# Performance work log

Hardware: AMD Instinct MI355X
Metric: run time of the kernel (lower is better)

The kernel has to match this reference:

```python
import jax, jax.numpy as jnp
import numpy as np

B, E, H, T = 32768, 64, 128, 12  # batch, embedding_dim, decoder_h_dim, pred_len


def setup_inputs() -> dict:
    key = jax.random.key(0)
    ks = jax.random.split(key, 13)
    f = lambda k, shape: jax.random.normal(k, shape, dtype=jnp.float32) * 0.05
    return {
        "last_pos": f(ks[0], (B, 2)),
        "last_pos_rel": f(ks[1], (B, 2)),
        "h0": f(ks[2], (1, B, H)),
        "c0": f(ks[3], (1, B, H)),
        "pred_ped_speed": jax.random.uniform(ks[4], (T, B, 1), dtype=jnp.float32),
        # spatial_embedding: Linear(3, E)
        "W_se": f(ks[5], (E, 3)),
        "b_se": f(ks[6], (E,)),
        # single-layer LSTM(E -> H), torch gate order [i, f, g, o]
        "W_ih": f(ks[7], (4 * H, E)),
        "W_hh": f(ks[8], (4 * H, H)),
        "b_ih": f(ks[9], (4 * H,)),
        "b_hh": f(ks[10], (4 * H,)),
        # hidden2pos: Linear(H, 2)
        "W_hp": f(ks[11], (2, H)),
        "b_hp": f(ks[12], (2,)),
    }


def reference(last_pos, last_pos_rel, h0, c0, pred_ped_speed,
              W_se, b_se, W_ih, W_hh, b_ih, b_hh, W_hp, b_hp):
    # train_or_test == 0 path: speed comes straight from pred_ped_speed
    Tlen = pred_ped_speed.shape[0]
    b_lstm = b_ih + b_hh
    # initial decoder input: embed concat([last_pos_rel, speed_0])  -> [B, E]
    x0 = jnp.concatenate([last_pos_rel, pred_ped_speed[0]], axis=1) @ W_se.T + b_se

    def step(carry, t):
        h, c, x, lp = carry  # h,c: [B,H]; x: [B,E]; lp: [B,2]
        gates = x @ W_ih.T + h @ W_hh.T + b_lstm           # [B, 4H]
        i, f_, g, o = jnp.split(gates, 4, axis=1)
        c = jax.nn.sigmoid(f_) * c + jax.nn.sigmoid(i) * jnp.tanh(g)
        h = jax.nn.sigmoid(o) * jnp.tanh(c)
        rel = h @ W_hp.T + b_hp                            # [B, 2]
        lp = rel + lp                                      # curr_pos -> last_pos
        # speed for next step; at final step torch keeps the previous speed
        spd = pred_ped_speed[jnp.minimum(t + 1, Tlen - 1)]
        x = jnp.concatenate([rel, spd], axis=1) @ W_se.T + b_se
        return (h, c, x, lp), rel

    (h, c, _, _), rels = jax.lax.scan(
        step, (h0[0], c0[0], x0, last_pos), jnp.arange(Tlen))
    # pred_traj_fake_rel: [T, B, 2]; final hidden state: [1, B, H]
    return rels, h[None]
```

## Files before the change

kernel.cpp:

```cpp
#include <hip/hip_runtime.h>

#define T_LEN 12
#define B_N   32768
#define H_N   128
#define BM    32

typedef __attribute__((ext_vector_type(8))) __bf16 bf16x8;
typedef __attribute__((ext_vector_type(8))) short  short8v;
typedef __attribute__((ext_vector_type(4))) float  f32x4;

__device__ __forceinline__ unsigned short f2bf(float f) {
  unsigned int u = __builtin_bit_cast(unsigned int, f);
  u += 0x7fffu + ((u >> 16) & 1u);
  return (unsigned short)(u >> 16);
}
__device__ __forceinline__ float sigm_p(float x) {
  return __builtin_amdgcn_rcpf(1.f + __builtin_amdgcn_exp2f(x));
}
__device__ __forceinline__ float tanh_p(float x) {
  return __builtin_fmaf(-2.f, __builtin_amdgcn_rcpf(__builtin_amdgcn_exp2f(x) + 1.f), 1.f);
}
__device__ __forceinline__ float tanh_c(float x) {
  return tanh_p(2.8853900817779268f * x);
}

__global__ void prep_kernel(const float* __restrict__ Wih, const float* __restrict__ Whh,
                            const float* __restrict__ bih, const float* __restrict__ bhh,
                            const float* __restrict__ Wse, const float* __restrict__ bse,
                            const float* __restrict__ Whp, const float* __restrict__ bhp,
                            unsigned short* __restrict__ WfA, unsigned short* __restrict__ pBg,
                            float* __restrict__ u, float* __restrict__ w0,
                            float* __restrict__ G) {
  const float SCL[4] = {-1.4426950408889634f, -1.4426950408889634f,
                         2.8853900817779268f, -1.4426950408889634f};
  int i = blockIdx.x * 256 + threadIdx.x;
  if (i < 65536) {
    int row = i >> 7, k = i & 127;
    float s = Whh[row * 128 + k];
    float wh0 = Whp[k], wh1 = Whp[128 + k];
    for (int e = 0; e < 64; ++e)
      s += Wih[row * 64 + e] * (Wse[e * 3 + 0] * wh0 + Wse[e * 3 + 1] * wh1);
    int g = row >> 7, unit = row & 127, w = unit >> 4, l15 = unit & 15;
    int ks = k >> 5, kg = (k >> 3) & 3, j = k & 7, l = kg * 16 + l15;
    WfA[((g * 4 + ks) * 512 + w * 64 + l) * 8 + j] = f2bf(s * SCL[g]);
  } else if (i < 65536 + 2048) {
    int j = i - 65536;
    int n = j >> 2, which = j & 3, g = n >> 7;
    float s = 0.f;
    if (which < 2) {
      for (int e = 0; e < 64; ++e) s += Wih[n * 64 + e] * Wse[e * 3 + which];
      G[n * 2 + which] = s * SCL[g];
    } else if (which == 2) {
      for (int e = 0; e < 64; ++e) s += Wih[n * 64 + e] * Wse[e * 3 + 2];
      u[n] = s * SCL[g];
    } else {
      for (int e = 0; e < 64; ++e)
        s += Wih[n * 64 + e] * (bse[e] + Wse[e * 3 + 0] * bhp[0] + Wse[e * 3 + 1] * bhp[1]);
      w0[n] = (bih[n] + bhh[n] + s) * SCL[g];
    }
  } else if (i < 65536 + 2048 + 2048) {
    int idx = i - 65536 - 2048;
    int ks = idx >> 9, l = (idx >> 3) & 63, j = idx & 7;
    int c = l & 15, kg = l >> 4;
    pBg[idx] = (c < 2) ? f2bf(Whp[c * 128 + ks * 32 + kg * 8 + j]) : (unsigned short)0;
  }
}

__launch_bounds__(512, 4)
__global__ void decoder_kernel(const float* __restrict__ lpr,
                               const float* __restrict__ h0,
                               const float* __restrict__ c0,
                               const float* __restrict__ pps,
                               const float* __restrict__ Whp,
                               const float* __restrict__ bhp,
                               const unsigned short* __restrict__ WfA,
                               const unsigned short* __restrict__ pBg,
                               const float* __restrict__ u,
                               const float* __restrict__ w0,
                               const float* __restrict__ G,
                               float* __restrict__ out_rel,
                               float* __restrict__ out_h) {
  __shared__ unsigned short hA[2][BM * 128];
  __shared__ unsigned short pBL[2048];
  __shared__ float spdL[T_LEN * BM];
  __shared__ float dbuf[BM * 2];
  __shared__ float GL[1024];

  const int tid  = threadIdx.x;
  const int wav  = tid >> 6;
  const int l    = tid & 63;
  const int l15  = l & 15;
  const int lg   = l >> 4;
  const int brow = blockIdx.x * BM;
  const int nh   = wav * 16 + l15;
  const int swzA = (l15 & 7) << 4;

  if (tid < 256) *(short8v*)(pBL + tid * 8) = *(const short8v*)(pBg + tid * 8);
  for (int i = tid; i < 1024; i += 512) GL[i] = G[i];
  if (tid < T_LEN * BM) spdL[tid] = pps[(tid >> 5) * B_N + brow + (tid & 31)];

  float w0r[4], ur[4];
#pragma unroll
  for (int g = 0; g < 4; ++g) { w0r[g] = w0[g * 128 + nh]; ur[g] = u[g * 128 + nh]; }

  f32x4 cst[2];
#pragma unroll
  for (int rt = 0; rt < 2; ++rt)
#pragma unroll
    for (int r = 0; r < 4; ++r)
      cst[rt][r] = c0[(brow + rt * 16 + lg * 4 + r) * H_N + nh];

  {
    int row = tid >> 4, k0 = (tid & 15) * 8;
    const float* src = h0 + (brow + row) * H_N + k0;
    unsigned short tmp[8];
#pragma unroll
    for (int j = 0; j < 8; ++j) tmp[j] = f2bf(src[j]);
    *(short8v*)((char*)&hA[0][0] + ((row * 256 + k0 * 2) ^ ((row & 7) << 4))) = *(short8v*)tmp;
  }
  {
    int dot = tid >> 3, part = tid & 7;
    int row = dot >> 1, jj = dot & 1;
    float s = 0.f;
    const float* hrow = h0 + (brow + row) * H_N + part * 16;
    const float* wrow = Whp + jj * 128 + part * 16;
#pragma unroll
    for (int k = 0; k < 16; ++k) s += hrow[k] * wrow[k];
    s += __shfl_xor(s, 1); s += __shfl_xor(s, 2); s += __shfl_xor(s, 4);
    if (part == 0) dbuf[dot] = lpr[(brow + row) * 2 + jj] - bhp[jj] - s;
  }
  const float bhpr = (l15 < 2) ? bhp[l15] : 0.f;

  char* rb = (char*)&hA[0][0];
  char* wbuf = (char*)&hA[1][0];

#pragma unroll 1
  for (int t = 0; t < T_LEN; ++t) {
    __syncthreads();

    f32x4 acc[4][2];
#pragma unroll
    for (int g = 0; g < 4; ++g)
#pragma unroll
      for (int rt = 0; rt < 2; ++rt)
        acc[g][rt] = (f32x4){w0r[g], w0r[g], w0r[g], w0r[g]};
    f32x4 relC = (f32x4){0.f, 0.f, 0.f, 0.f};

#pragma unroll
    for (int ks = 0; ks < 4; ++ks) {
      const int kk = (ks + t) & 3;
      bf16x8 a0 = __builtin_bit_cast(bf16x8,
          *(short8v*)(rb + ((l15 * 256 + kk * 64 + lg * 16) ^ swzA)));
      bf16x8 a1 = __builtin_bit_cast(bf16x8,
          *(short8v*)(rb + (((16 + l15) * 256 + kk * 64 + lg * 16) ^ swzA)));
      bf16x8 b0 = __builtin_bit_cast(bf16x8, *(const short8v*)(WfA + ((0 * 4 + kk) * 512 + wav * 64 + l) * 8));
      bf16x8 b1 = __builtin_bit_cast(bf16x8, *(const short8v*)(WfA + ((1 * 4 + kk) * 512 + wav * 64 + l) * 8));
      bf16x8 b2 = __builtin_bit_cast(bf16x8, *(const short8v*)(WfA + ((2 * 4 + kk) * 512 + wav * 64 + l) * 8));
      bf16x8 b3 = __builtin_bit_cast(bf16x8, *(const short8v*)(WfA + ((3 * 4 + kk) * 512 + wav * 64 + l) * 8));
      acc[0][0] = __builtin_amdgcn_mfma_f32_16x16x32_bf16(a0, b0, acc[0][0], 0, 0, 0);
      acc[0][1] = __builtin_amdgcn_mfma_f32_16x16x32_bf16(a1, b0, acc[0][1], 0, 0, 0);
      acc[1][0] = __builtin_amdgcn_mfma_f32_16x16x32_bf16(a0, b1, acc[1][0], 0, 0, 0);
      acc[1][1] = __builtin_amdgcn_mfma_f32_16x16x32_bf16(a1, b1, acc[1][1], 0, 0, 0);
      acc[2][0] = __builtin_amdgcn_mfma_f32_16x16x32_bf16(a0, b2, acc[2][0], 0, 0, 0);
      acc[2][1] = __builtin_amdgcn_mfma_f32_16x16x32_bf16(a1, b2, acc[2][1], 0, 0, 0);
      acc[3][0] = __builtin_amdgcn_mfma_f32_16x16x32_bf16(a0, b3, acc[3][0], 0, 0, 0);
      acc[3][1] = __builtin_amdgcn_mfma_f32_16x16x32_bf16(a1, b3, acc[3][1], 0, 0, 0);
      if (wav < 2 && t > 0) {
        bf16x8 pb = __builtin_bit_cast(bf16x8, *(short8v*)(pBL + (kk * 64 + l) * 8));
        relC = __builtin_amdgcn_mfma_f32_16x16x32_bf16(wav == 0 ? a0 : a1, pb, relC, 0, 0, 0);
      }
    }
    if (wav < 2 && t > 0 && l15 < 2) {
#pragma unroll
      for (int r = 0; r < 4; ++r)
        out_rel[(size_t)(t - 1) * B_N * 2 + (brow + wav * 16 + lg * 4 + r) * 2 + l15] = relC[r] + bhpr;
    }

#pragma unroll
    for (int rt = 0; rt < 2; ++rt) {
      const f32x4 spdv = *(const f32x4*)(spdL + t * BM + rt * 16 + lg * 4);
      if (t == 0) {
#pragma unroll
        for (int r = 0; r < 4; ++r) {
          int row = rt * 16 + lg * 4 + r;
          float d0 = dbuf[row * 2 + 0], d1 = dbuf[row * 2 + 1];
#pragma unroll
          for (int g = 0; g < 4; ++g)
            acc[g][rt][r] += d0 * GL[(g * 128 + nh) * 2 + 0] + d1 * GL[(g * 128 + nh) * 2 + 1];
        }
      }
#pragma unroll
      for (int r = 0; r < 4; ++r) {
        int row = rt * 16 + lg * 4 + r;
        float spd = spdv[r];
        float gi = __builtin_fmaf(spd, ur[0], acc[0][rt][r]);
        float gf = __builtin_fmaf(spd, ur[1], acc[1][rt][r]);
        float gg = __builtin_fmaf(spd, ur[2], acc[2][rt][r]);
        float go = __builtin_fmaf(spd, ur[3], acc[3][rt][r]);
        float cn = sigm_p(gf) * cst[rt][r] + sigm_p(gi) * tanh_p(gg);
        cst[rt][r] = cn;
        float h = sigm_p(go) * tanh_c(cn);
        *(unsigned short*)(wbuf + ((row * 256 + nh * 2) ^ ((row & 7) << 4))) = f2bf(h);
        if (t == T_LEN - 1) out_h[(brow + row) * H_N + nh] = h;
      }
    }
    char* tmpp = rb; rb = wbuf; wbuf = tmpp;
  }

  __syncthreads();
  if (wav < 2) {
    f32x4 relC = (f32x4){0.f, 0.f, 0.f, 0.f};
#pragma unroll
    for (int ks = 0; ks < 4; ++ks) {
      bf16x8 a = __builtin_bit_cast(bf16x8,
          *(short8v*)(rb + (((wav * 16 + l15) * 256 + ks * 64 + lg * 16) ^ swzA)));
      bf16x8 pb = __builtin_bit_cast(bf16x8, *(short8v*)(pBL + (ks * 64 + l) * 8));
      relC = __builtin_amdgcn_mfma_f32_16x16x32_bf16(a, pb, relC, 0, 0, 0);
    }
    if (l15 < 2) {
#pragma unroll
      for (int r = 0; r < 4; ++r)
        out_rel[(size_t)(T_LEN - 1) * B_N * 2 + (brow + wav * 16 + lg * 4 + r) * 2 + l15] = relC[r] + bhpr;
    }
  }
}

extern "C" void kernel_launch(void* const* d_in, const int* in_sizes, int n_in,
                              void* d_out, int out_size, void* d_ws, size_t ws_size,
                              hipStream_t stream) {
  const float* lpr  = (const float*)d_in[1];
  const float* h0   = (const float*)d_in[2];
  const float* c0   = (const float*)d_in[3];
  const float* pps  = (const float*)d_in[4];
  const float* W_se = (const float*)d_in[5];
  const float* b_se = (const float*)d_in[6];
  const float* W_ih = (const float*)d_in[7];
  const float* W_hh = (const float*)d_in[8];
  const float* b_ih = (const float*)d_in[9];
  const float* b_hh = (const float*)d_in[10];
  const float* W_hp = (const float*)d_in[11];
  const float* b_hp = (const float*)d_in[12];

  unsigned short* WfA = (unsigned short*)d_ws;
  unsigned short* pBg = (unsigned short*)((char*)d_ws + 131072);
  float* u  = (float*)((char*)d_ws + 135168);
  float* w0 = (float*)((char*)d_ws + 137216);
  float* G  = (float*)((char*)d_ws + 139264);

  float* out_rel = (float*)d_out;
  float* out_h   = out_rel + (size_t)T_LEN * B_N * 2;

  hipLaunchKernelGGL(prep_kernel, dim3((65536 + 4096 + 255) / 256), dim3(256), 0, stream,
                     W_ih, W_hh, b_ih, b_hh, W_se, b_se, W_hp, b_hp,
                     WfA, pBg, u, w0, G);
  hipLaunchKernelGGL(decoder_kernel, dim3(B_N / BM), dim3(512), 0, stream,
                     lpr, h0, c0, pps, W_hp, b_hp, WfA, pBg, u, w0, G,
                     out_rel, out_h);
}
```

Baseline: 217.3 us.

## Double batch rows per block and process them in two sequential passes

Raises the batch tile from 32 to 64 rows per block. Each timestep now runs two passes of 32 rows, so every wave reuses the same weight-load pattern across both passes. Initial loads, the hidden-to-pos dot, the rel output wave mapping and the final epilogue are adjusted to cover 64 rows. This halves the grid and amortizes per-block setup and synchronization, but doubles the cell-state registers and LDS footprint, which can lower occupancy.

Result: slower. 431.8 us (+98.7%).

```diff
diff --git a/kernel.cpp b/kernel.cpp
--- a/kernel.cpp
+++ b/kernel.cpp
@@ -3,7 +3,7 @@
 #define T_LEN 12
 #define B_N   32768
 #define H_N   128
-#define BM    32
+#define BM    64
 
 typedef __attribute__((ext_vector_type(8))) __bf16 bf16x8;
 typedef __attribute__((ext_vector_type(8))) short  short8v;
@@ -97,21 +97,24 @@
 
   if (tid < 256) *(short8v*)(pBL + tid * 8) = *(const short8v*)(pBg + tid * 8);
   for (int i = tid; i < 1024; i += 512) GL[i] = G[i];
-  if (tid < T_LEN * BM) spdL[tid] = pps[(tid >> 5) * B_N + brow + (tid & 31)];
+  for (int i = tid; i < T_LEN * BM; i += 512)
+    spdL[i] = pps[(i >> 6) * B_N + brow + (i & 63)];
 
   float w0r[4], ur[4];
 #pragma unroll
   for (int g = 0; g < 4; ++g) { w0r[g] = w0[g * 128 + nh]; ur[g] = u[g * 128 + nh]; }
 
-  f32x4 cst[2];
-#pragma unroll
-  for (int rt = 0; rt < 2; ++rt)
+  f32x4 cst[4];
+#pragma unroll
+  for (int rt = 0; rt < 4; ++rt)
 #pragma unroll
     for (int r = 0; r < 4; ++r)
       cst[rt][r] = c0[(brow + rt * 16 + lg * 4 + r) * H_N + nh];
 
-  {
-    int row = tid >> 4, k0 = (tid & 15) * 8;
+#pragma unroll
+  for (int it = 0; it < 2; ++it) {
+    int idx = it * 512 + tid;
+    int row = idx >> 4, k0 = (idx & 15) * 8;
     const float* src = h0 + (brow + row) * H_N + k0;
     unsigned short tmp[8];
 #pragma unroll
@@ -119,14 +122,14 @@
     *(short8v*)((char*)&hA[0][0] + ((row * 256 + k0 * 2) ^ ((row & 7) << 4))) = *(short8v*)tmp;
   }
   {
-    int dot = tid >> 3, part = tid & 7;
+    int dot = tid >> 2, part = tid & 3;
     int row = dot >> 1, jj = dot & 1;
     float s = 0.f;
-    const float* hrow = h0 + (brow + row) * H_N + part * 16;
-    const float* wrow = Whp + jj * 128 + part * 16;
-#pragma unroll
-    for (int k = 0; k < 16; ++k) s += hrow[k] * wrow[k];
-    s += __shfl_xor(s, 1); s += __shfl_xor(s, 2); s += __shfl_xor(s, 4);
+    const float* hrow = h0 + (brow + row) * H_N + part * 32;
+    const float* wrow = Whp + jj * 128 + part * 32;
+#pragma unroll
+    for (int k = 0; k < 32; ++k) s += hrow[k] * wrow[k];
+    s += __shfl_xor(s, 1); s += __shfl_xor(s, 2);
     if (part == 0) dbuf[dot] = lpr[(brow + row) * 2 + jj] - bhp[jj] - s;
   }
   const float bhpr = (l15 < 2) ? bhp[l15] : 0.f;
@@ -138,77 +141,82 @@
   for (int t = 0; t < T_LEN; ++t) {
     __syncthreads();
 
-    f32x4 acc[4][2];
-#pragma unroll
-    for (int g = 0; g < 4; ++g)
-#pragma unroll
-      for (int rt = 0; rt < 2; ++rt)
-        acc[g][rt] = (f32x4){w0r[g], w0r[g], w0r[g], w0r[g]};
-    f32x4 relC = (f32x4){0.f, 0.f, 0.f, 0.f};
-
-#pragma unroll
-    for (int ks = 0; ks < 4; ++ks) {
-      const int kk = (ks + t) & 3;
-      bf16x8 a0 = __builtin_bit_cast(bf16x8,
-          *(short8v*)(rb + ((l15 * 256 + kk * 64 + lg * 16) ^ swzA)));
-      bf16x8 a1 = __builtin_bit_cast(bf16x8,
-          *(short8v*)(rb + (((16 + l15) * 256 + kk * 64 + lg * 16) ^ swzA)));
-      bf16x8 b0 = __builtin_bit_cast(bf16x8, *(const short8v*)(WfA + ((0 * 4 + kk) * 512 + wav * 64 + l) * 8));
-      bf16x8 b1 = __builtin_bit_cast(bf16x8, *(const short8v*)(WfA + ((1 * 4 + kk) * 512 + wav * 64 + l) * 8));
-      bf16x8 b2 = __builtin_bit_cast(bf16x8, *(const short8v*)(WfA + ((2 * 4 + kk) * 512 + wav * 64 + l) * 8));
-      bf16x8 b3 = __builtin_bit_cast(bf16x8, *(const short8v*)(WfA + ((3 * 4 + kk) * 512 + wav * 64 + l) * 8));
-      acc[0][0] = __builtin_amdgcn_mfma_f32_16x16x32_bf16(a0, b0, acc[0][0], 0, 0, 0);
-      acc[0][1] = __builtin_amdgcn_mfma_f32_16x16x32_bf16(a1, b0, acc[0][1], 0, 0, 0);
-      acc[1][0] = __builtin_amdgcn_mfma_f32_16x16x32_bf16(a0, b1, acc[1][0], 0, 0, 0);
-      acc[1][1] = __builtin_amdgcn_mfma_f32_16x16x32_bf16(a1, b1, acc[1][1], 0, 0, 0);
-      acc[2][0] = __builtin_amdgcn_mfma_f32_16x16x32_bf16(a0, b2, acc[2][0], 0, 0, 0);
-      acc[2][1] = __builtin_amdgcn_mfma_f32_16x16x32_bf16(a1, b2, acc[2][1], 0, 0, 0);
-      acc[3][0] = __builtin_amdgcn_mfma_f32_16x16x32_bf16(a0, b3, acc[3][0], 0, 0, 0);
-      acc[3][1] = __builtin_amdgcn_mfma_f32_16x16x32_bf16(a1, b3, acc[3][1], 0, 0, 0);
-      if (wav < 2 && t > 0) {
-        bf16x8 pb = __builtin_bit_cast(bf16x8, *(short8v*)(pBL + (kk * 64 + l) * 8));
-        relC = __builtin_amdgcn_mfma_f32_16x16x32_bf16(wav == 0 ? a0 : a1, pb, relC, 0, 0, 0);
+#pragma unroll
+    for (int p = 0; p < 2; ++p) {
+      f32x4 acc[4][2];
+#pragma unroll
+      for (int g = 0; g < 4; ++g)
+#pragma unroll
+        for (int h2 = 0; h2 < 2; ++h2)
+          acc[g][h2] = (f32x4){w0r[g], w0r[g], w0r[g], w0r[g]};
+      f32x4 relC = (f32x4){0.f, 0.f, 0.f, 0.f};
+      const bool relw = ((wav >> 1) == p);
+
+#pragma unroll
+      for (int ks = 0; ks < 4; ++ks) {
+        const int kk = (ks + t) & 3;
+        bf16x8 a0 = __builtin_bit_cast(bf16x8,
+            *(short8v*)(rb + (((p * 32 + l15) * 256 + kk * 64 + lg * 16) ^ swzA)));
+        bf16x8 a1 = __builtin_bit_cast(bf16x8,
+            *(short8v*)(rb + (((p * 32 + 16 + l15) * 256 + kk * 64 + lg * 16) ^ swzA)));
+        bf16x8 b0 = __builtin_bit_cast(bf16x8, *(const short8v*)(WfA + ((0 * 4 + kk) * 512 + wav * 64 + l) * 8));
+        bf16x8 b1 = __builtin_bit_cast(bf16x8, *(const short8v*)(WfA + ((1 * 4 + kk) * 512 + wav * 64 + l) * 8));
+        bf16x8 b2 = __builtin_bit_cast(bf16x8, *(const short8v*)(WfA + ((2 * 4 + kk) * 512 + wav * 64 + l) * 8));
+        bf16x8 b3 = __builtin_bit_cast(bf16x8, *(const short8v*)(WfA + ((3 * 4 + kk) * 512 + wav * 64 + l) * 8));
+        acc[0][0] = __builtin_amdgcn_mfma_f32_16x16x32_bf16(a0, b0, acc[0][0], 0, 0, 0);
+        acc[0][1] = __builtin_amdgcn_mfma_f32_16x16x32_bf16(a1, b0, acc[0][1], 0, 0, 0);
+        acc[1][0] = __builtin_amdgcn_mfma_f32_16x16x32_bf16(a0, b1, acc[1][0], 0, 0, 0);
+        acc[1][1] = __builtin_amdgcn_mfma_f32_16x16x32_bf16(a1, b1, acc[1][1], 0, 0, 0);
+        acc[2][0] = __builtin_amdgcn_mfma_f32_16x16x32_bf16(a0, b2, acc[2][0], 0, 0, 0);
+        acc[2][1] = __builtin_amdgcn_mfma_f32_16x16x32_bf16(a1, b2, acc[2][1], 0, 0, 0);
+        acc[3][0] = __builtin_amdgcn_mfma_f32_16x16x32_bf16(a0, b3, acc[3][0], 0, 0, 0);
+        acc[3][1] = __builtin_amdgcn_mfma_f32_16x16x32_bf16(a1, b3, acc[3][1], 0, 0, 0);
+        if (relw && t > 0) {
+          bf16x8 pb = __builtin_bit_cast(bf16x8, *(short8v*)(pBL + (kk * 64 + l) * 8));
+          relC = __builtin_amdgcn_mfma_f32_16x16x32_bf16((wav & 1) ? a1 : a0, pb, relC, 0, 0, 0);
+        }
       }
-    }
-    if (wav < 2 && t > 0 && l15 < 2) {
-#pragma unroll
-      for (int r = 0; r < 4; ++r)
-        out_rel[(size_t)(t - 1) * B_N * 2 + (brow + wav * 16 + lg * 4 + r) * 2 + l15] = relC[r] + bhpr;
-    }
-
-#pragma unroll
-    for (int rt = 0; rt < 2; ++rt) {
-      const f32x4 spdv = *(const f32x4*)(spdL + t * BM + rt * 16 + lg * 4);
-      if (t == 0) {
+      if (relw && t > 0 && l15 < 2) {
+#pragma unroll
+        for (int r = 0; r < 4; ++r)
+          out_rel[(size_t)(t - 1) * B_N * 2 + (brow + wav * 16 + lg * 4 + r) * 2 + l15] = relC[r] + bhpr;
+      }
+
+#pragma unroll
+      for (int h2 = 0; h2 < 2; ++h2) {
+        const int rt = p * 2 + h2;
+        const f32x4 spdv = *(const f32x4*)(spdL + t * BM + rt * 16 + lg * 4);
+        if (t == 0) {
+#pragma unroll
+          for (int r = 0; r < 4; ++r) {
+            int row = rt * 16 + lg * 4 + r;
+            float d0 = dbuf[row * 2 + 0], d1 = dbuf[row * 2 + 1];
+#pragma unroll
+            for (int g = 0; g < 4; ++g)
+              acc[g][h2][r] += d0 * GL[(g * 128 + nh) * 2 + 0] + d1 * GL[(g * 128 + nh) * 2 + 1];
+          }
+        }
 #pragma unroll
         for (int r = 0; r < 4; ++r) {
           int row = rt * 16 + lg * 4 + r;
-          float d0 = dbuf[row * 2 + 0], d1 = dbuf[row * 2 + 1];
-#pragma unroll
-          for (int g = 0; g < 4; ++g)
-            acc[g][rt][r] += d0 * GL[(g * 128 + nh) * 2 + 0] + d1 * GL[(g * 128 + nh) * 2 + 1];
+          float spd = spdv[r];
+          float gi = __builtin_fmaf(spd, ur[0], acc[0][h2][r]);
+          float gf = __builtin_fmaf(spd, ur[1], acc[1][h2][r]);
+          float gg = __builtin_fmaf(spd, ur[2], acc[2][h2][r]);
+          float go = __builtin_fmaf(spd, ur[3], acc[3][h2][r]);
+          float cn = sigm_p(gf) * cst[rt][r] + sigm_p(gi) * tanh_p(gg);
+          cst[rt][r] = cn;
+          float h = sigm_p(go) * tanh_c(cn);
+          *(unsigned short*)(wbuf + ((row * 256 + nh * 2) ^ ((row & 7) << 4))) = f2bf(h);
+          if (t == T_LEN - 1) out_h[(brow + row) * H_N + nh] = h;
         }
       }
-#pragma unroll
-      for (int r = 0; r < 4; ++r) {
-        int row = rt * 16 + lg * 4 + r;
-        float spd = spdv[r];
-        float gi = __builtin_fmaf(spd, ur[0], acc[0][rt][r]);
-        float gf = __builtin_fmaf(spd, ur[1], acc[1][rt][r]);
-        float gg = __builtin_fmaf(spd, ur[2], acc[2][rt][r]);
-        float go = __builtin_fmaf(spd, ur[3], acc[3][rt][r]);
-        float cn = sigm_p(gf) * cst[rt][r] + sigm_p(gi) * tanh_p(gg);
-        cst[rt][r] = cn;
-        float h = sigm_p(go) * tanh_c(cn);
-        *(unsigned short*)(wbuf + ((row * 256 + nh * 2) ^ ((row & 7) << 4))) = f2bf(h);
-        if (t == T_LEN - 1) out_h[(brow + row) * H_N + nh] = h;
-      }
     }
     char* tmpp = rb; rb = wbuf; wbuf = tmpp;
   }
 
   __syncthreads();
-  if (wav < 2) {
+  if (wav < 4) {
     f32x4 relC = (f32x4){0.f, 0.f, 0.f, 0.f};
 #pragma unroll
     for (int ks = 0; ks < 4; ++ks) {
```
